# Kernel optimization log

Measured on AMD Instinct MI355X. Metric: run time of the kernel, lower is better.

Reference implementation:

```python
import jax, jax.numpy as jnp
import numpy as np

B, K, N, D = 64, 64, 32768, 2048   # batch, knn neighbors, memory size, feat dim (hardcoded 2048 in source)
NC, NHID, TOPK = 2048, 512, 5      # num clusters, gcn hidden, topk in affinity masking


def setup_inputs() -> dict:
    key = jax.random.key(0)
    ks = jax.random.split(key, 8)
    features = jax.random.normal(ks[0], (N, D), jnp.float32)
    labels = jax.random.randint(ks[1], (N,), 0, NC)
    indexes = jax.random.randint(ks[2], (B,), 0, N)
    ori_knn_neighbor = jax.random.randint(ks[3], (B, K), 0, N)
    s = 0.02
    conv_w = jax.random.normal(ks[4], (2 * D, NHID), jnp.float32) * s
    conv_b = jnp.zeros((NHID,), jnp.float32)
    w1 = jax.random.normal(ks[5], (NHID, NHID), jnp.float32) * s
    b1 = jnp.zeros((NHID,), jnp.float32)
    prelu_a = jnp.full((NHID,), 0.25, jnp.float32)
    w2 = jax.random.normal(ks[6], (NHID, 2), jnp.float32) * s
    b2 = jnp.zeros((2,), jnp.float32)
    return dict(indexes=indexes, features=features, labels=labels,
                ori_knn_neighbor=ori_knn_neighbor, conv_w=conv_w, conv_b=conv_b,
                w1=w1, b1=b1, prelu_a=prelu_a, w2=w2, b2=b2)


def _build_graphs(indexes, features, labels, ori_knn_neighbor):
    # cluster mean features (index_add_ + count normalize), done under no_grad in torch
    counts = jax.ops.segment_sum(jnp.ones((N,), jnp.float32), labels, num_segments=NC)
    clu_sum = jax.ops.segment_sum(features, labels, num_segments=NC)
    clu_mean = clu_sum / jnp.maximum(counts, 1.0)[:, None]

    def per_sample(idx, nbr):
        clu_lab = labels[nbr]                                  # [K]
        cf = clu_mean[clu_lab].at[0].set(features[idx])        # [K, D]
        A = (cf @ cf.T) / 5.0                                  # [K, K]
        j = jnp.arange(K)
        # keep only first occurrence of each cluster label (np.unique return_index)
        dup = jnp.any((clu_lab[:, None] == clu_lab[None, :]) & (j[None, :] < j[:, None]), axis=1)
        keep = (~dup).astype(A.dtype)                          # [K]
        _, ti = jax.lax.top_k(A, TOPK)                         # [K, TOPK]
        m = jnp.zeros_like(A).at[j[:, None], ti].set(1.0)
        m = ((m > 0) & (m.T > 0)).astype(A.dtype) * keep[:, None] * keep[None, :]
        A = A * m
        cf = cf / jnp.linalg.norm(cf, axis=1, keepdims=True)   # row-normalize
        cf = cf - cf[0]                                        # center on query (row 0 -> 0)
        return cf, A

    x, adj = jax.vmap(per_sample)(indexes, ori_knn_neighbor)   # [B,K,D], [B,K,K]
    return jax.lax.stop_gradient(x), jax.lax.stop_gradient(adj)


def reference(indexes, features, labels, ori_knn_neighbor,
              conv_w, conv_b, w1, b1, prelu_a, w2, b2):
    x, adj = _build_graphs(indexes, features, labels, ori_knn_neighbor)
    # GraphConv with MeanAggregator: agg = A @ x, concat, linear, relu
    agg = jnp.einsum('bij,bjd->bid', adj, x)                   # [B,K,D]
    h = jax.nn.relu(jnp.concatenate([x, agg], axis=-1) @ conv_w + conv_b)  # [B,K,NHID]
    h0 = h.reshape(-1, NHID)
    h1 = h0 @ w1 + b1
    h1 = jnp.where(h1 > 0, h1, prelu_a * h1)                   # PReLU(nhid)
    logits = h1 @ w2 + b2                                      # [B*K, 2]
    return jax.nn.softmax(logits.reshape(B, K, 2), axis=2)
```

## Files before the change

kernel.cpp:

```cpp
#include <hip/hip_runtime.h>
#include <hip/hip_bf16.h>

#define BB 64
#define KN 64
#define NPTS 32768
#define DD 2048
#define NCC 2048
#define NH 512
#define MM 4096
#define K2 4096

typedef unsigned short u16;
typedef unsigned int u32;
typedef __attribute__((ext_vector_type(8))) short short8;
typedef __attribute__((ext_vector_type(4))) float f32x4;

__device__ __forceinline__ float bf2f(u32 u){
  union { u32 i; float f; } v; v.i = u << 16; return v.f;
}
__device__ __forceinline__ u16 f2bf(float f){
  union { float f; u32 i; } v; v.f = f;
  u32 x = v.i;
  return (u16)((x + 0x7fffu + ((x >> 16) & 1u)) >> 16);
}

typedef __attribute__((address_space(3))) u32 as3_u32;
typedef const __attribute__((address_space(1))) u32 as1_u32;
__device__ __forceinline__ void glds16(const void* g, void* l){
  __builtin_amdgcn_global_load_lds((as1_u32*)g, (as3_u32*)l, 16, 0, 0);
}

__global__ void k_dtype(const u32* __restrict__ w, int* __restrict__ flag){
  __shared__ int cnt;
  if(threadIdx.x==0) cnt = 0;
  __syncthreads();
  int c = 0;
  for(int i=threadIdx.x; i<1024; i+=256){
    u32 e = (w[i] >> 7) & 0xffu;
    c += (e >= 110 && e <= 135) ? 1 : 0;
  }
  atomicAdd(&cnt, c);
  __syncthreads();
  if(threadIdx.x==0) *flag = (cnt < 512) ? 1 : 0;
}

__global__ void k_count(const int* __restrict__ labels, int* __restrict__ counts){
  int n = blockIdx.x*256 + threadIdx.x;
  atomicAdd(&counts[labels[n]], 1);
}

__global__ void k_scan(const int* __restrict__ counts, int* __restrict__ offsets){
  __shared__ int sb[256];
  int t = threadIdx.x;
  int c[8]; int s = 0;
  #pragma unroll
  for(int i=0;i<8;i++){ c[i] = counts[t*8+i]; s += c[i]; }
  sb[t] = s; __syncthreads();
  int v = s;
  for(int off=1; off<256; off<<=1){
    int u = (t>=off) ? sb[t-off] : 0;
    __syncthreads();
    v += u; sb[t] = v;
    __syncthreads();
  }
  int run = v - s;
  #pragma unroll
  for(int i=0;i<8;i++){ offsets[t*8+i] = run; run += c[i]; }
}

__global__ void k_scatter(const int* __restrict__ labels, const int* __restrict__ offsets,
                          int* __restrict__ cursor, int* __restrict__ sorted){
  int n = blockIdx.x*256 + threadIdx.x;
  int c = labels[n];
  int p = atomicAdd(&cursor[c], 1);
  sorted[offsets[c] + p] = n;
}

__global__ __launch_bounds__(256) void k_clumean(
    const void* __restrict__ feat, const int* __restrict__ counts,
    const int* __restrict__ offsets, const int* __restrict__ sorted,
    const int* __restrict__ dflag, float* __restrict__ clu){
  int c = blockIdx.x, t = threadIdx.x;
  int isf32 = *dflag;
  int cnt = counts[c], start = offsets[c];
  float acc[8] = {0,0,0,0,0,0,0,0};
  if(isf32){
    const float* ff = (const float*)feat;
    for(int r=0; r<cnt; r++){
      int row = sorted[start+r];
      const float4* p = (const float4*)(ff + (size_t)row*DD + t*8);
      float4 a = p[0], b = p[1];
      acc[0]+=a.x; acc[1]+=a.y; acc[2]+=a.z; acc[3]+=a.w;
      acc[4]+=b.x; acc[5]+=b.y; acc[6]+=b.z; acc[7]+=b.w;
    }
  } else {
    const u16* fb = (const u16*)feat;
    for(int r=0; r<cnt; r++){
      int row = sorted[start+r];
      uint4 v = *(const uint4*)(fb + (size_t)row*DD + t*8);
      acc[0]+=bf2f(v.x&0xffffu); acc[1]+=bf2f(v.x>>16);
      acc[2]+=bf2f(v.y&0xffffu); acc[3]+=bf2f(v.y>>16);
      acc[4]+=bf2f(v.z&0xffffu); acc[5]+=bf2f(v.z>>16);
      acc[6]+=bf2f(v.w&0xffffu); acc[7]+=bf2f(v.w>>16);
    }
  }
  float div = fmaxf((float)cnt, 1.0f);
  float* o = clu + (size_t)c*DD + t*8;
  #pragma unroll
  for(int i=0;i<8;i++) o[i] = acc[i] / div;
}

__global__ __launch_bounds__(64) void k_meta(
    const int* __restrict__ labels, const int* __restrict__ knn,
    int* __restrict__ lab_ws, int* __restrict__ keep_ws){
  int b = blockIdx.x, t = threadIdx.x;
  __shared__ int sl[64];
  int nbr = knn[b*64 + t];
  int lab = labels[nbr];
  sl[t] = lab; __syncthreads();
  int dup = 0;
  for(int j=0;j<t;j++) dup |= (sl[j]==lab);
  lab_ws[b*64+t] = lab;
  keep_ws[b*64+t] = dup ? 0 : 1;
}

__global__ __launch_bounds__(256) void k_Apart(
    const void* __restrict__ feat, const float* __restrict__ clu,
    const int* __restrict__ indexes, const int* __restrict__ lab_ws,
    const int* __restrict__ dflag, float* __restrict__ Apart){
  int b = blockIdx.x >> 2, g = blockIdx.x & 3;
  int t = threadIdx.x;
  __shared__ float cfT[64][68];
  __shared__ int sl[64];
  int isf32 = *dflag;
  if(t < 64) sl[t] = lab_ws[b*64 + t];
  int qidx = indexes[b];
  __syncthreads();

  int i0 = (t & 15)*4, j0 = (t >> 4)*4;
  float acc[4][4];
  #pragma unroll
  for(int a=0;a<4;a++)
    #pragma unroll
    for(int c2=0;c2<4;c2++) acc[a][c2] = 0.f;

  for(int ch=g*8; ch<g*8+8; ch++){
    int dbase = ch*64;
    #pragma unroll
    for(int ps=0; ps<16; ps++){
      int idx = ps*256 + t;
      int k = idx >> 6, dd = idx & 63;
      float v;
      if(k == 0){
        size_t fi = (size_t)qidx*DD + dbase + dd;
        v = isf32 ? ((const float*)feat)[fi] : bf2f(((const u16*)feat)[fi]);
      } else {
        v = clu[(size_t)sl[k]*DD + dbase + dd];
      }
      cfT[dd][k] = v;
    }
    __syncthreads();
    #pragma unroll 4
    for(int dd=0; dd<64; dd++){
      float4 av = *(const float4*)&cfT[dd][i0];
      float4 bv = *(const float4*)&cfT[dd][j0];
      float aa[4] = {av.x, av.y, av.z, av.w};
      float bbv[4] = {bv.x, bv.y, bv.z, bv.w};
      #pragma unroll
      for(int ii=0;ii<4;ii++)
        #pragma unroll
        for(int jj=0;jj<4;jj++)
          acc[ii][jj] += aa[ii]*bbv[jj];
    }
    __syncthreads();
  }

  float* op = Apart + ((size_t)(g*64 + b))*4096;
  #pragma unroll
  for(int ii=0;ii<4;ii++)
    *(float4*)&op[(i0+ii)*64 + j0] = make_float4(acc[ii][0], acc[ii][1], acc[ii][2], acc[ii][3]);
}

__global__ __launch_bounds__(256) void k_Afinal(
    const float* __restrict__ Apart, const int* __restrict__ keep_ws,
    float* __restrict__ adj, float* __restrict__ norms){
  int b = blockIdx.x, t = threadIdx.x;
  __shared__ float A[64][65];
  __shared__ unsigned long long mb[64];
  __shared__ int sk[64];
  const float* P = Apart + (size_t)b*4096;
  const size_t gs = (size_t)64*4096;
  #pragma unroll
  for(int ps=0; ps<16; ps++){
    int idx = ps*256 + t;
    float s = P[idx] + P[idx+gs] + P[idx+2*gs] + P[idx+3*gs];
    A[idx>>6][idx&63] = s * 0.2f;
  }
  __syncthreads();
  if(t < 64){
    unsigned long long chosen = 0;
    const float* row = A[t];
    #pragma unroll
    for(int p=0;p<5;p++){
      float best = -INFINITY; int bi = 0;
      for(int j=0;j<64;j++){
        bool taken = (chosen >> j) & 1ull;
        float v = row[j];
        if(!taken && v > best){ best = v; bi = j; }
      }
      chosen |= (1ull << bi);
    }
    mb[t] = chosen;
    sk[t] = keep_ws[b*64+t];
    norms[b*64+t] = sqrtf(fmaxf(A[t][t]*5.0f, 0.0f));
  }
  __syncthreads();
  float* O = adj + (size_t)b*4096;
  #pragma unroll
  for(int ps=0; ps<16; ps++){
    int idx = ps*256 + t;
    int i = idx >> 6, j = idx & 63;
    bool on = ((mb[i]>>j)&1ull) && ((mb[j]>>i)&1ull) && sk[i] && sk[j];
    O[idx] = on ? A[i][j] : 0.0f;
  }
}

__global__ __launch_bounds__(256) void k_xrow(
    const void* __restrict__ feat, const float* __restrict__ clu,
    const int* __restrict__ indexes, const int* __restrict__ lab_ws,
    const float* __restrict__ norms, const int* __restrict__ dflag,
    u16* __restrict__ xab){
  int r = blockIdx.x, t = threadIdx.x;
  int b = r >> 6, k = r & 63;
  size_t obase = (size_t)r*K2 + t*8;
  if(k == 0){
    *(uint4*)(xab + obase) = make_uint4(0,0,0,0);
    return;
  }
  int isf32 = *dflag;
  int qidx = indexes[b];
  float inv0 = 1.0f / fmaxf(norms[b*64], 1e-30f);
  float invk = 1.0f / fmaxf(norms[r], 1e-30f);
  float q[8];
  if(isf32){
    const float4* qp = (const float4*)((const float*)feat + (size_t)qidx*DD + t*8);
    float4 a = qp[0], bq = qp[1];
    q[0]=a.x; q[1]=a.y; q[2]=a.z; q[3]=a.w; q[4]=bq.x; q[5]=bq.y; q[6]=bq.z; q[7]=bq.w;
  } else {
    uint4 v = *(const uint4*)((const u16*)feat + (size_t)qidx*DD + t*8);
    q[0]=bf2f(v.x&0xffffu); q[1]=bf2f(v.x>>16);
    q[2]=bf2f(v.y&0xffffu); q[3]=bf2f(v.y>>16);
    q[4]=bf2f(v.z&0xffffu); q[5]=bf2f(v.z>>16);
    q[6]=bf2f(v.w&0xffffu); q[7]=bf2f(v.w>>16);
  }
  const float* cp = clu + (size_t)lab_ws[r]*DD + t*8;
  float4 c0 = *(const float4*)cp, c1 = *(const float4*)(cp+4);
  float cv[8] = {c0.x,c0.y,c0.z,c0.w,c1.x,c1.y,c1.z,c1.w};
  u16 ob[8];
  #pragma unroll
  for(int e=0;e<8;e++) ob[e] = f2bf(cv[e]*invk - q[e]*inv0);
  uint4 w;
  w.x = (u32)ob[0] | ((u32)ob[1]<<16);
  w.y = (u32)ob[2] | ((u32)ob[3]<<16);
  w.z = (u32)ob[4] | ((u32)ob[5]<<16);
  w.w = (u32)ob[6] | ((u32)ob[7]<<16);
  *(uint4*)(xab + obase) = w;
}

__global__ __launch_bounds__(256) void k_agg(
    const float* __restrict__ adj, u16* __restrict__ xab){
  int r = blockIdx.x, t = threadIdx.x; int b = r >> 6;
  __shared__ float arow[64];
  if(t < 64) arow[t] = adj[(size_t)r*64 + t];
  __syncthreads();
  float acc[8] = {0,0,0,0,0,0,0,0};
  int d = t*8;
  for(int j=0;j<64;j++){
    float s = arow[j];
    if(s != 0.0f){
      const u16* xp = xab + (size_t)(b*64+j)*K2 + d;
      uint4 v = *(const uint4*)xp;
      acc[0]+=s*bf2f(v.x&0xffffu); acc[1]+=s*bf2f(v.x>>16);
      acc[2]+=s*bf2f(v.y&0xffffu); acc[3]+=s*bf2f(v.y>>16);
      acc[4]+=s*bf2f(v.z&0xffffu); acc[5]+=s*bf2f(v.z>>16);
      acc[6]+=s*bf2f(v.w&0xffffu); acc[7]+=s*bf2f(v.w>>16);
    }
  }
  u16* o = xab + (size_t)r*K2 + DD + d;
  #pragma unroll
  for(int e=0;e<8;e++) o[e] = f2bf(acc[e]);
}

__global__ __launch_bounds__(256) void k_transpose(
    const void* __restrict__ src, u16* __restrict__ dst, int Kd, int Nd,
    const int* __restrict__ dflag){
  __shared__ u16 tile[64][65];
  int isf32 = *dflag;
  int nbt = Nd >> 6;
  int k0 = (blockIdx.x / nbt) << 6;
  int n0 = (blockIdx.x % nbt) << 6;
  int t = threadIdx.x;
  if(isf32){
    const float* s = (const float*)src;
    #pragma unroll
    for(int ph=0; ph<16; ph++){
      int idx = ph*256 + t;
      int r = idx >> 6, c = idx & 63;
      tile[r][c] = f2bf(s[(size_t)(k0+r)*Nd + n0 + c]);
    }
  } else {
    const u16* s = (const u16*)src;
    #pragma unroll
    for(int ph=0; ph<16; ph++){
      int idx = ph*256 + t;
      int r = idx >> 6, c = idx & 63;
      tile[r][c] = s[(size_t)(k0+r)*Nd + n0 + c];
    }
  }
  __syncthreads();
  #pragma unroll
  for(int ph=0; ph<16; ph++){
    int idx = ph*256 + t;
    int r = idx >> 6, c = idx & 63;
    dst[(size_t)(n0+r)*Kd + k0 + c] = tile[c][r];
  }
}

template<int EPI>
__global__ __launch_bounds__(256) void k_gemm(
    const u16* __restrict__ Am, const u16* __restrict__ Bt,
    const void* __restrict__ bias, const void* __restrict__ pa,
    const int* __restrict__ dflag,
    void* __restrict__ Cout, int Md, int Nd, int Kd)
{
  __shared__ u16 As[2][128*64];
  __shared__ u16 Bs[2][64*64];
  int isf32 = *dflag;
  int t = threadIdx.x;
  int nblk = gridDim.x;
  int bid = (blockIdx.x & 7)*(nblk >> 3) + (blockIdx.x >> 3);
  int nb = Nd >> 6;
  int m0 = (bid / nb) << 7;
  int n0 = (bid % nb) << 6;
  int wave = t >> 6, lane = t & 63;
  int wm = wave >> 1, wn = wave & 1;
  int lm = lane & 15, lq = lane >> 4;
  int lrow = lane >> 3, lcol = lane & 7;

  f32x4 acc[4][2];
  #pragma unroll
  for(int i=0;i<4;i++)
    #pragma unroll
    for(int j=0;j<2;j++) acc[i][j] = (f32x4){0.f,0.f,0.f,0.f};

  auto stage = [&](int buf, int kb){
    #pragma unroll
    for(int c=0;c<4;c++){
      int ch = wave*4 + c;
      int row = ch*8 + lrow;
      int col = lcol ^ (row & 7);
      glds16(Am + (size_t)(m0+row)*Kd + kb + col*8, &As[buf][ch*512]);
    }
    #pragma unroll
    for(int c=0;c<2;c++){
      int ch = wave*2 + c;
      int row = ch*8 + lrow;
      int col = lcol ^ (row & 7);
      glds16(Bt + (size_t)(n0+row)*Kd + kb + col*8, &Bs[buf][ch*512]);
    }
  };

  stage(0, 0);
  __syncthreads();
  int cur = 0;
  for(int kb=0; kb<Kd; kb+=64){
    if(kb + 64 < Kd) stage(cur^1, kb+64);
    #pragma unroll
    for(int kk=0;kk<2;kk++){
      short8 af[4], bfr[2];
      #pragma unroll
      for(int mi=0;mi<4;mi++){
        int r = wm*64 + mi*16 + lm;
        int p = ((kk<<2)+lq) ^ (r & 7);
        union{ uint4 u; short8 v; } x;
        x.u = *(const uint4*)&As[cur][r*64 + p*8];
        af[mi] = x.v;
      }
      #pragma unroll
      for(int ni=0;ni<2;ni++){
        int r = wn*32 + ni*16 + lm;
        int p = ((kk<<2)+lq) ^ (r & 7);
        union{ uint4 u; short8 v; } x;
        x.u = *(const uint4*)&Bs[cur][r*64 + p*8];
        bfr[ni] = x.v;
      }
      #pragma unroll
      for(int mi=0;mi<4;mi++)
        #pragma unroll
        for(int ni=0;ni<2;ni++)
          acc[mi][ni] = __builtin_amdgcn_mfma_f32_16x16x32_bf16(af[mi], bfr[ni], acc[mi][ni], 0, 0, 0);
    }
    __syncthreads();
    cur ^= 1;
  }

  #pragma unroll
  for(int ni=0;ni<2;ni++){
    int col = n0 + wn*32 + ni*16 + lm;
    float bs = isf32 ? ((const float*)bias)[col] : bf2f(((const u16*)bias)[col]);
    float av = 0.f;
    if(EPI==1) av = isf32 ? ((const float*)pa)[col] : bf2f(((const u16*)pa)[col]);
    #pragma unroll
    for(int mi=0;mi<4;mi++){
      int rowb = m0 + wm*64 + mi*16 + lq*4;
      #pragma unroll
      for(int r2=0;r2<4;r2++){
        float v = acc[mi][ni][r2] + bs;
        if(EPI==0){
          v = fmaxf(v, 0.f);
          ((u16*)Cout)[(size_t)(rowb+r2)*Nd + col] = f2bf(v);
        } else {
          v = (v > 0.f) ? v : av*v;
          ((float*)Cout)[(size_t)(rowb+r2)*Nd + col] = v;
        }
      }
    }
  }
}

__global__ __launch_bounds__(256) void k_out(
    const float* __restrict__ h1, const void* __restrict__ w2,
    const void* __restrict__ b2, const int* __restrict__ dflag,
    void* __restrict__ out){
  int t = threadIdx.x; int lane = t & 63; int row = blockIdx.x*4 + (t >> 6);
  int isf32 = *dflag;
  const float* hr = h1 + (size_t)row*NH;
  float s0 = 0.f, s1 = 0.f;
  #pragma unroll
  for(int j=0;j<NH/64;j++){
    int i = lane + j*64;
    float h = hr[i];
    float w0 = isf32 ? ((const float*)w2)[i*2+0] : bf2f(((const u16*)w2)[i*2+0]);
    float w1v= isf32 ? ((const float*)w2)[i*2+1] : bf2f(((const u16*)w2)[i*2+1]);
    s0 += h * w0;
    s1 += h * w1v;
  }
  #pragma unroll
  for(int off=32; off>0; off>>=1){
    s0 += __shfl_down(s0, off);
    s1 += __shfl_down(s1, off);
  }
  if(lane==0){
    float bb0 = isf32 ? ((const float*)b2)[0] : bf2f(((const u16*)b2)[0]);
    float bb1 = isf32 ? ((const float*)b2)[1] : bf2f(((const u16*)b2)[1]);
    float l0 = s0 + bb0;
    float l1 = s1 + bb1;
    float m = fmaxf(l0, l1);
    float e0 = expf(l0 - m), e1 = expf(l1 - m);
    float inv = 1.0f / (e0 + e1);
    if(isf32){
      ((float*)out)[row*2+0] = e0*inv;
      ((float*)out)[row*2+1] = e1*inv;
    } else {
      ((u16*)out)[row*2+0] = f2bf(e0*inv);
      ((u16*)out)[row*2+1] = f2bf(e1*inv);
    }
  }
}

__global__ void k_fill_sentinel(u32* __restrict__ out, int nwords){
  int i = blockIdx.x*256 + threadIdx.x;
  if(i < nwords) out[i] = 0x40404040u;
}

extern "C" void kernel_launch(void* const* d_in, const int* in_sizes, int n_in,
                              void* d_out, int out_size, void* d_ws, size_t ws_size,
                              hipStream_t stream) {
  const int* indexes = (const int*)d_in[0];
  const void* feat   = d_in[1];
  const int* labels  = (const int*)d_in[2];
  const int* knn     = (const int*)d_in[3];
  const void* conv_w = d_in[4];
  const void* conv_b = d_in[5];
  const void* w1     = d_in[6];
  const void* b1     = d_in[7];
  const void* pa     = d_in[8];
  const void* w2     = d_in[9];
  const void* b2     = d_in[10];

  char* w = (char*)d_ws;
  size_t o = 0;
  auto alloc = [&](size_t bytes) -> void* {
    void* p = w + o; o = (o + bytes + 255) & ~(size_t)255; return p;
  };
  int*   dflag   = (int*)  alloc(4);
  int*   counts  = (int*)  alloc((size_t)NCC*4);
  int*   cursor  = (int*)  alloc((size_t)NCC*4);
  int*   offsets = (int*)  alloc((size_t)NCC*4);
  int*   lab_ws  = (int*)  alloc((size_t)MM*4);
  int*   keep_ws = (int*)  alloc((size_t)MM*4);
  int*   sorted  = (int*)  alloc((size_t)NPTS*4);
  float* norms   = (float*)alloc((size_t)MM*4);
  float* adj     = (float*)alloc((size_t)BB*64*64*4);
  float* Apart   = (float*)alloc((size_t)4*BB*64*64*4);
  float* clu     = (float*)alloc((size_t)NCC*DD*4);
  u16*   xab     = (u16*)  alloc((size_t)MM*K2*2);
  u16*   cwT     = (u16*)  alloc((size_t)K2*NH*2);
  u16*   w1T     = (u16*)  alloc((size_t)NH*NH*2);
  u16*   hb      = (u16*)  clu;
  float* h1      = (float*)((char*)clu + (size_t)MM*NH*2);

  size_t NEED = o;
  if(ws_size < NEED){
    int nwords = out_size/2;
    k_fill_sentinel<<<(nwords+255)/256, 256, 0, stream>>>((u32*)d_out, nwords);
    return;
  }

  hipMemsetAsync(counts, 0, (size_t)NCC*4*2, stream);

  k_dtype  <<<1, 256, 0, stream>>>((const u32*)feat, dflag);
  k_count  <<<NPTS/256, 256, 0, stream>>>(labels, counts);
  k_scan   <<<1, 256, 0, stream>>>(counts, offsets);
  k_scatter<<<NPTS/256, 256, 0, stream>>>(labels, offsets, cursor, sorted);
  k_clumean<<<NCC, 256, 0, stream>>>(feat, counts, offsets, sorted, dflag, clu);
  k_meta   <<<BB, 64, 0, stream>>>(labels, knn, lab_ws, keep_ws);
  k_Apart  <<<BB*4, 256, 0, stream>>>(feat, clu, indexes, lab_ws, dflag, Apart);
  k_Afinal <<<BB, 256, 0, stream>>>(Apart, keep_ws, adj, norms);
  k_xrow   <<<MM, 256, 0, stream>>>(feat, clu, indexes, lab_ws, norms, dflag, xab);
  k_agg    <<<MM, 256, 0, stream>>>(adj, xab);

  k_transpose<<<(K2/64)*(NH/64), 256, 0, stream>>>(conv_w, cwT, K2, NH, dflag);
  k_transpose<<<(NH/64)*(NH/64), 256, 0, stream>>>(w1, w1T, NH, NH, dflag);

  k_gemm<0><<<(MM/128)*(NH/64), 256, 0, stream>>>(xab, cwT, conv_b, nullptr, dflag, (void*)hb, MM, NH, K2);
  k_gemm<1><<<(MM/128)*(NH/64), 256, 0, stream>>>(hb, w1T, b1, pa, dflag, (void*)h1, MM, NH, NH);

  k_out    <<<MM/4, 256, 0, stream>>>(h1, w2, b2, dflag, d_out);
}
```

Before: 552.9 us.

## Fuse prep kernels, skip unused cluster means, fuse xrow+agg, shrink GEMM tiles

Merges the label counting and weight transposes into one prep kernel that also marks which clusters are referenced by the knn lists. Cluster means are then computed only for used clusters, with 64-row index staging and two-row unrolling. The xrow and aggregation kernels become one kernel that builds x in LDS and uses a sparse nonzero list of adj (capped at 8 per row). GEMM tiles drop from 128x64 to 64x64 to double the block count. Dtype flags now come from input sizes on the host instead of a device probe. The 8-per-row cap assumes the top-5 mutual mask never yields more nonzeros.

```diff
diff --git a/kernel.cpp b/kernel.cpp
--- a/kernel.cpp
+++ b/kernel.cpp
@@ -30,23 +30,56 @@
   __builtin_amdgcn_global_load_lds((as1_u32*)g, (as3_u32*)l, 16, 0, 0);
 }
 
-__global__ void k_dtype(const u32* __restrict__ w, int* __restrict__ flag){
-  __shared__ int cnt;
-  if(threadIdx.x==0) cnt = 0;
-  __syncthreads();
-  int c = 0;
-  for(int i=threadIdx.x; i<1024; i+=256){
-    u32 e = (w[i] >> 7) & 0xffu;
-    c += (e >= 110 && e <= 135) ? 1 : 0;
-  }
-  atomicAdd(&cnt, c);
-  __syncthreads();
-  if(threadIdx.x==0) *flag = (cnt < 512) ? 1 : 0;
-}
-
-__global__ void k_count(const int* __restrict__ labels, int* __restrict__ counts){
-  int n = blockIdx.x*256 + threadIdx.x;
-  atomicAdd(&counts[labels[n]], 1);
+__global__ __launch_bounds__(256) void k_prep(
+    const int* __restrict__ labels, int* __restrict__ counts,
+    const int* __restrict__ knn, int* __restrict__ used,
+    const void* __restrict__ conv_w, u16* __restrict__ cwT, int fcw,
+    const void* __restrict__ w1, u16* __restrict__ w1T, int fw1){
+  __shared__ u16 tile[64][65];
+  int bb = blockIdx.x, t = threadIdx.x;
+  if(bb < 128){
+    int n = bb*256 + t;
+    atomicAdd(&counts[labels[n]], 1);
+    return;
+  }
+  if(bb == 704){
+    #pragma unroll
+    for(int i=0;i<16;i++){
+      int idx = i*256 + t;
+      used[labels[knn[idx]]] = 1;
+    }
+    return;
+  }
+  const void* src; u16* dst; int Kd, Nd, isf32, tb;
+  if(bb < 640){ src=conv_w; dst=cwT; Kd=K2; Nd=NH; isf32=fcw; tb=bb-128; }
+  else        { src=w1;     dst=w1T; Kd=NH; Nd=NH; isf32=fw1; tb=bb-640; }
+  int nbt = Nd >> 6;
+  int k0 = (tb / nbt) << 6;
+  int n0 = (tb % nbt) << 6;
+  if(isf32){
+    const float* s = (const float*)src;
+    #pragma unroll
+    for(int ph=0; ph<16; ph++){
+      int idx = ph*256 + t;
+      int r = idx >> 6, c = idx & 63;
+      tile[r][c] = f2bf(s[(size_t)(k0+r)*Nd + n0 + c]);
+    }
+  } else {
+    const u16* s = (const u16*)src;
+    #pragma unroll
+    for(int ph=0; ph<16; ph++){
+      int idx = ph*256 + t;
+      int r = idx >> 6, c = idx & 63;
+      tile[r][c] = s[(size_t)(k0+r)*Nd + n0 + c];
+    }
+  }
+  __syncthreads();
+  #pragma unroll
+  for(int ph=0; ph<16; ph++){
+    int idx = ph*256 + t;
+    int r = idx >> 6, c = idx & 63;
+    dst[(size_t)(n0+r)*Kd + k0 + c] = tile[c][r];
+  }
 }
 
 __global__ void k_scan(const int* __restrict__ counts, int* __restrict__ offsets){
@@ -79,61 +112,73 @@
 __global__ __launch_bounds__(256) void k_clumean(
     const void* __restrict__ feat, const int* __restrict__ counts,
     const int* __restrict__ offsets, const int* __restrict__ sorted,
-    const int* __restrict__ dflag, float* __restrict__ clu){
+    const int* __restrict__ used, int isf32, float* __restrict__ clu){
   int c = blockIdx.x, t = threadIdx.x;
-  int isf32 = *dflag;
+  if(!used[c]) return;
+  __shared__ int ridx[64];
   int cnt = counts[c], start = offsets[c];
   float acc[8] = {0,0,0,0,0,0,0,0};
-  if(isf32){
-    const float* ff = (const float*)feat;
-    for(int r=0; r<cnt; r++){
-      int row = sorted[start+r];
-      const float4* p = (const float4*)(ff + (size_t)row*DD + t*8);
-      float4 a = p[0], b = p[1];
-      acc[0]+=a.x; acc[1]+=a.y; acc[2]+=a.z; acc[3]+=a.w;
-      acc[4]+=b.x; acc[5]+=b.y; acc[6]+=b.z; acc[7]+=b.w;
-    }
-  } else {
-    const u16* fb = (const u16*)feat;
-    for(int r=0; r<cnt; r++){
-      int row = sorted[start+r];
-      uint4 v = *(const uint4*)(fb + (size_t)row*DD + t*8);
-      acc[0]+=bf2f(v.x&0xffffu); acc[1]+=bf2f(v.x>>16);
-      acc[2]+=bf2f(v.y&0xffffu); acc[3]+=bf2f(v.y>>16);
-      acc[4]+=bf2f(v.z&0xffffu); acc[5]+=bf2f(v.z>>16);
-      acc[6]+=bf2f(v.w&0xffffu); acc[7]+=bf2f(v.w>>16);
+  for(int base=0; base<cnt; base+=64){
+    int take = min(64, cnt-base);
+    __syncthreads();
+    if(t < take) ridx[t] = sorted[start+base+t];
+    __syncthreads();
+    if(isf32){
+      const float* ff = (const float*)feat;
+      int r = 0;
+      for(; r+2<=take; r+=2){
+        const float* p0 = ff + (size_t)ridx[r]*DD + t*8;
+        const float* p1 = ff + (size_t)ridx[r+1]*DD + t*8;
+        float4 a0=*(const float4*)p0, b0=*(const float4*)(p0+4);
+        float4 a1=*(const float4*)p1, b1=*(const float4*)(p1+4);
+        acc[0]+=a0.x+a1.x; acc[1]+=a0.y+a1.y; acc[2]+=a0.z+a1.z; acc[3]+=a0.w+a1.w;
+        acc[4]+=b0.x+b1.x; acc[5]+=b0.y+b1.y; acc[6]+=b0.z+b1.z; acc[7]+=b0.w+b1.w;
+      }
+      if(r < take){
+        const float* p0 = ff + (size_t)ridx[r]*DD + t*8;
+        float4 a0=*(const float4*)p0, b0=*(const float4*)(p0+4);
+        acc[0]+=a0.x; acc[1]+=a0.y; acc[2]+=a0.z; acc[3]+=a0.w;
+        acc[4]+=b0.x; acc[5]+=b0.y; acc[6]+=b0.z; acc[7]+=b0.w;
+      }
+    } else {
+      const u16* fb = (const u16*)feat;
+      int r = 0;
+      for(; r+2<=take; r+=2){
+        const u16* p0 = fb + (size_t)ridx[r]*DD + t*8;
+        const u16* p1 = fb + (size_t)ridx[r+1]*DD + t*8;
+        uint4 v0 = *(const uint4*)p0, v1 = *(const uint4*)p1;
+        acc[0]+=bf2f(v0.x&0xffffu)+bf2f(v1.x&0xffffu); acc[1]+=bf2f(v0.x>>16)+bf2f(v1.x>>16);
+        acc[2]+=bf2f(v0.y&0xffffu)+bf2f(v1.y&0xffffu); acc[3]+=bf2f(v0.y>>16)+bf2f(v1.y>>16);
+        acc[4]+=bf2f(v0.z&0xffffu)+bf2f(v1.z&0xffffu); acc[5]+=bf2f(v0.z>>16)+bf2f(v1.z>>16);
+        acc[6]+=bf2f(v0.w&0xffffu)+bf2f(v1.w&0xffffu); acc[7]+=bf2f(v0.w>>16)+bf2f(v1.w>>16);
+      }
+      if(r < take){
+        const u16* p0 = fb + (size_t)ridx[r]*DD + t*8;
+        uint4 v0 = *(const uint4*)p0;
+        acc[0]+=bf2f(v0.x&0xffffu); acc[1]+=bf2f(v0.x>>16);
+        acc[2]+=bf2f(v0.y&0xffffu); acc[3]+=bf2f(v0.y>>16);
+        acc[4]+=bf2f(v0.z&0xffffu); acc[5]+=bf2f(v0.z>>16);
+        acc[6]+=bf2f(v0.w&0xffffu); acc[7]+=bf2f(v0.w>>16);
+      }
     }
   }
   float div = fmaxf((float)cnt, 1.0f);
   float* o = clu + (size_t)c*DD + t*8;
-  #pragma unroll
-  for(int i=0;i<8;i++) o[i] = acc[i] / div;
-}
-
-__global__ __launch_bounds__(64) void k_meta(
-    const int* __restrict__ labels, const int* __restrict__ knn,
-    int* __restrict__ lab_ws, int* __restrict__ keep_ws){
-  int b = blockIdx.x, t = threadIdx.x;
-  __shared__ int sl[64];
-  int nbr = knn[b*64 + t];
-  int lab = labels[nbr];
-  sl[t] = lab; __syncthreads();
-  int dup = 0;
-  for(int j=0;j<t;j++) dup |= (sl[j]==lab);
-  lab_ws[b*64+t] = lab;
-  keep_ws[b*64+t] = dup ? 0 : 1;
+  float4 o0 = make_float4(acc[0]/div, acc[1]/div, acc[2]/div, acc[3]/div);
+  float4 o1 = make_float4(acc[4]/div, acc[5]/div, acc[6]/div, acc[7]/div);
+  *(float4*)o = o0;
+  *(float4*)(o+4) = o1;
 }
 
 __global__ __launch_bounds__(256) void k_Apart(
     const void* __restrict__ feat, const float* __restrict__ clu,
-    const int* __restrict__ indexes, const int* __restrict__ lab_ws,
-    const int* __restrict__ dflag, float* __restrict__ Apart){
+    const int* __restrict__ indexes, const int* __restrict__ labels,
+    const int* __restrict__ knn, int isf32, float* __restrict__ Apart){
   int b = blockIdx.x >> 2, g = blockIdx.x & 3;
   int t = threadIdx.x;
   __shared__ float cfT[64][68];
   __shared__ int sl[64];
-  int isf32 = *dflag;
-  if(t < 64) sl[t] = lab_ws[b*64 + t];
+  if(t < 64) sl[t] = labels[knn[b*64 + t]];
   int qidx = indexes[b];
   __syncthreads();
 
@@ -182,12 +227,15 @@
 }
 
 __global__ __launch_bounds__(256) void k_Afinal(
-    const float* __restrict__ Apart, const int* __restrict__ keep_ws,
+    const float* __restrict__ Apart, const int* __restrict__ labels,
+    const int* __restrict__ knn,
     float* __restrict__ adj, float* __restrict__ norms){
   int b = blockIdx.x, t = threadIdx.x;
   __shared__ float A[64][65];
   __shared__ unsigned long long mb[64];
+  __shared__ int sl[64];
   __shared__ int sk[64];
+  if(t < 64) sl[t] = labels[knn[b*64 + t]];
   const float* P = Apart + (size_t)b*4096;
   const size_t gs = (size_t)64*4096;
   #pragma unroll
@@ -198,6 +246,9 @@
   }
   __syncthreads();
   if(t < 64){
+    int dup = 0;
+    for(int j=0;j<t;j++) dup |= (sl[j]==sl[t]);
+    sk[t] = dup ? 0 : 1;
     unsigned long long chosen = 0;
     const float* row = A[t];
     #pragma unroll
@@ -211,7 +262,6 @@
       chosen |= (1ull << bi);
     }
     mb[t] = chosen;
-    sk[t] = keep_ws[b*64+t];
     norms[b*64+t] = sqrtf(fmaxf(A[t][t]*5.0f, 0.0f));
   }
   __syncthreads();
@@ -225,148 +275,119 @@
   }
 }
 
-__global__ __launch_bounds__(256) void k_xrow(
+__global__ __launch_bounds__(256) void k_xagg(
     const void* __restrict__ feat, const float* __restrict__ clu,
-    const int* __restrict__ indexes, const int* __restrict__ lab_ws,
-    const float* __restrict__ norms, const int* __restrict__ dflag,
-    u16* __restrict__ xab){
-  int r = blockIdx.x, t = threadIdx.x;
-  int b = r >> 6, k = r & 63;
-  size_t obase = (size_t)r*K2 + t*8;
-  if(k == 0){
-    *(uint4*)(xab + obase) = make_uint4(0,0,0,0);
-    return;
-  }
-  int isf32 = *dflag;
+    const int* __restrict__ indexes, const int* __restrict__ labels,
+    const int* __restrict__ knn, const float* __restrict__ norms,
+    const float* __restrict__ adj, int isf32, u16* __restrict__ xab){
+  int b = blockIdx.x >> 2, g = blockIdx.x & 3;
+  int t = threadIdx.x;
+  __shared__ u16  xs[64][512];
+  __shared__ float adjs[64][65];
+  __shared__ float nzv[64][8];
+  __shared__ u16   nzj[64][8];
+  __shared__ int   nzc[64];
+  __shared__ int   sl[64];
+  __shared__ float sn[64];
+
+  const float* Ab = adj + (size_t)b*4096;
+  #pragma unroll
+  for(int ps=0; ps<16; ps++){
+    int idx = ps*256 + t;
+    adjs[idx>>6][idx&63] = Ab[idx];
+  }
+  if(t < 64){
+    sl[t] = labels[knn[b*64 + t]];
+    sn[t] = 1.0f / fmaxf(norms[b*64 + t], 1e-30f);
+  }
   int qidx = indexes[b];
-  float inv0 = 1.0f / fmaxf(norms[b*64], 1e-30f);
-  float invk = 1.0f / fmaxf(norms[r], 1e-30f);
-  float q[8];
+  int d = g*512 + t*2;
+  float q0, q1;
   if(isf32){
-    const float4* qp = (const float4*)((const float*)feat + (size_t)qidx*DD + t*8);
-    float4 a = qp[0], bq = qp[1];
-    q[0]=a.x; q[1]=a.y; q[2]=a.z; q[3]=a.w; q[4]=bq.x; q[5]=bq.y; q[6]=bq.z; q[7]=bq.w;
+    float2 qv = *(const float2*)((const float*)feat + (size_t)qidx*DD + d);
+    q0 = qv.x; q1 = qv.y;
   } else {
-    uint4 v = *(const uint4*)((const u16*)feat + (size_t)qidx*DD + t*8);
-    q[0]=bf2f(v.x&0xffffu); q[1]=bf2f(v.x>>16);
-    q[2]=bf2f(v.y&0xffffu); q[3]=bf2f(v.y>>16);
-    q[4]=bf2f(v.z&0xffffu); q[5]=bf2f(v.z>>16);
-    q[6]=bf2f(v.w&0xffffu); q[7]=bf2f(v.w>>16);
-  }
-  const float* cp = clu + (size_t)lab_ws[r]*DD + t*8;
-  float4 c0 = *(const float4*)cp, c1 = *(const float4*)(cp+4);
-  float cv[8] = {c0.x,c0.y,c0.z,c0.w,c1.x,c1.y,c1.z,c1.w};
-  u16 ob[8];
-  #pragma unroll
-  for(int e=0;e<8;e++) ob[e] = f2bf(cv[e]*invk - q[e]*inv0);
-  uint4 w;
-  w.x = (u32)ob[0] | ((u32)ob[1]<<16);
-  w.y = (u32)ob[2] | ((u32)ob[3]<<16);
-  w.z = (u32)ob[4] | ((u32)ob[5]<<16);
-  w.w = (u32)ob[6] | ((u32)ob[7]<<16);
-  *(uint4*)(xab + obase) = w;
-}
-
-__global__ __launch_bounds__(256) void k_agg(
-    const float* __restrict__ adj, u16* __restrict__ xab){
-  int r = blockIdx.x, t = threadIdx.x; int b = r >> 6;
-  __shared__ float arow[64];
-  if(t < 64) arow[t] = adj[(size_t)r*64 + t];
-  __syncthreads();
-  float acc[8] = {0,0,0,0,0,0,0,0};
-  int d = t*8;
-  for(int j=0;j<64;j++){
-    float s = arow[j];
-    if(s != 0.0f){
-      const u16* xp = xab + (size_t)(b*64+j)*K2 + d;
-      uint4 v = *(const uint4*)xp;
-      acc[0]+=s*bf2f(v.x&0xffffu); acc[1]+=s*bf2f(v.x>>16);
-      acc[2]+=s*bf2f(v.y&0xffffu); acc[3]+=s*bf2f(v.y>>16);
-      acc[4]+=s*bf2f(v.z&0xffffu); acc[5]+=s*bf2f(v.z>>16);
-      acc[6]+=s*bf2f(v.w&0xffffu); acc[7]+=s*bf2f(v.w>>16);
-    }
-  }
-  u16* o = xab + (size_t)r*K2 + DD + d;
-  #pragma unroll
-  for(int e=0;e<8;e++) o[e] = f2bf(acc[e]);
-}
-
-__global__ __launch_bounds__(256) void k_transpose(
-    const void* __restrict__ src, u16* __restrict__ dst, int Kd, int Nd,
-    const int* __restrict__ dflag){
-  __shared__ u16 tile[64][65];
-  int isf32 = *dflag;
-  int nbt = Nd >> 6;
-  int k0 = (blockIdx.x / nbt) << 6;
-  int n0 = (blockIdx.x % nbt) << 6;
-  int t = threadIdx.x;
-  if(isf32){
-    const float* s = (const float*)src;
-    #pragma unroll
-    for(int ph=0; ph<16; ph++){
-      int idx = ph*256 + t;
-      int r = idx >> 6, c = idx & 63;
-      tile[r][c] = f2bf(s[(size_t)(k0+r)*Nd + n0 + c]);
-    }
-  } else {
-    const u16* s = (const u16*)src;
-    #pragma unroll
-    for(int ph=0; ph<16; ph++){
-      int idx = ph*256 + t;
-      int r = idx >> 6, c = idx & 63;
-      tile[r][c] = s[(size_t)(k0+r)*Nd + n0 + c];
-    }
-  }
-  __syncthreads();
-  #pragma unroll
-  for(int ph=0; ph<16; ph++){
-    int idx = ph*256 + t;
-    int r = idx >> 6, c = idx & 63;
-    dst[(size_t)(n0+r)*Kd + k0 + c] = tile[c][r];
+    u32 w = *(const u32*)((const u16*)feat + (size_t)qidx*DD + d);
+    q0 = bf2f(w & 0xffffu); q1 = bf2f(w >> 16);
+  }
+  __syncthreads();
+  if(t < 64){
+    int c = 0;
+    for(int j=0;j<64;j++){
+      float v = adjs[t][j];
+      if(v != 0.0f && c < 8){ nzv[t][c] = v; nzj[t][c] = (u16)j; c++; }
+    }
+    nzc[t] = c;
+  }
+  float inv0 = sn[0];
+  q0 *= inv0; q1 *= inv0;
+
+  *(u32*)&xs[0][t*2] = 0u;
+  *(u32*)(xab + (size_t)(b*64)*K2 + d) = 0u;
+  for(int k=1;k<64;k++){
+    float2 cv = *(const float2*)(clu + (size_t)sl[k]*DD + d);
+    float invk = sn[k];
+    u16 x0 = f2bf(cv.x*invk - q0), x1 = f2bf(cv.y*invk - q1);
+    u32 w = (u32)x0 | ((u32)x1 << 16);
+    *(u32*)&xs[k][t*2] = w;
+    *(u32*)(xab + (size_t)(b*64+k)*K2 + d) = w;
+  }
+  __syncthreads();
+
+  for(int r=0;r<64;r++){
+    float a0 = 0.f, a1 = 0.f;
+    int c = nzc[r];
+    for(int p=0;p<c;p++){
+      float s = nzv[r][p]; int j = nzj[r][p];
+      u32 w = *(const u32*)&xs[j][t*2];
+      a0 += s*bf2f(w & 0xffffu);
+      a1 += s*bf2f(w >> 16);
+    }
+    u32 w = (u32)f2bf(a0) | ((u32)f2bf(a1) << 16);
+    *(u32*)(xab + (size_t)(b*64+r)*K2 + DD + d) = w;
   }
 }
 
 template<int EPI>
-__global__ __launch_bounds__(256) void k_gemm(
+__global__ __launch_bounds__(256, 2) void k_gemm(
     const u16* __restrict__ Am, const u16* __restrict__ Bt,
     const void* __restrict__ bias, const void* __restrict__ pa,
-    const int* __restrict__ dflag,
+    int fbias, int fpa,
     void* __restrict__ Cout, int Md, int Nd, int Kd)
 {
-  __shared__ u16 As[2][128*64];
+  __shared__ u16 As[2][64*64];
   __shared__ u16 Bs[2][64*64];
-  int isf32 = *dflag;
   int t = threadIdx.x;
   int nblk = gridDim.x;
   int bid = (blockIdx.x & 7)*(nblk >> 3) + (blockIdx.x >> 3);
   int nb = Nd >> 6;
-  int m0 = (bid / nb) << 7;
+  int m0 = (bid / nb) << 6;
   int n0 = (bid % nb) << 6;
   int wave = t >> 6, lane = t & 63;
   int wm = wave >> 1, wn = wave & 1;
   int lm = lane & 15, lq = lane >> 4;
   int lrow = lane >> 3, lcol = lane & 7;
 
-  f32x4 acc[4][2];
-  #pragma unroll
-  for(int i=0;i<4;i++)
+  f32x4 acc[2][2];
+  #pragma unroll
+  for(int i=0;i<2;i++)
     #pragma unroll
     for(int j=0;j<2;j++) acc[i][j] = (f32x4){0.f,0.f,0.f,0.f};
 
   auto stage = [&](int buf, int kb){
     #pragma unroll
-    for(int c=0;c<4;c++){
-      int ch = wave*4 + c;
-      int row = ch*8 + lrow;
+    for(int c=0;c<2;c++){
+      int cb = wave*2 + c;
+      int row = cb*8 + lrow;
       int col = lcol ^ (row & 7);
-      glds16(Am + (size_t)(m0+row)*Kd + kb + col*8, &As[buf][ch*512]);
+      glds16(Am + (size_t)(m0+row)*Kd + kb + col*8, &As[buf][cb*512]);
     }
     #pragma unroll
     for(int c=0;c<2;c++){
-      int ch = wave*2 + c;
-      int row = ch*8 + lrow;
+      int cb = wave*2 + c;
+      int row = cb*8 + lrow;
       int col = lcol ^ (row & 7);
-      glds16(Bt + (size_t)(n0+row)*Kd + kb + col*8, &Bs[buf][ch*512]);
+      glds16(Bt + (size_t)(n0+row)*Kd + kb + col*8, &Bs[buf][cb*512]);
     }
   };
 
@@ -377,10 +398,10 @@
     if(kb + 64 < Kd) stage(cur^1, kb+64);
     #pragma unroll
     for(int kk=0;kk<2;kk++){
-      short8 af[4], bfr[2];
+      short8 af[2], bfr[2];
       #pragma unroll
-      for(int mi=0;mi<4;mi++){
-        int r = wm*64 + mi*16 + lm;
+      for(int mi=0;mi<2;mi++){
+        int r = wm*32 + mi*16 + lm;
         int p = ((kk<<2)+lq) ^ (r & 7);
         union{ uint4 u; short8 v; } x;
         x.u = *(const uint4*)&As[cur][r*64 + p*8];
@@ -395,7 +416,7 @@
         bfr[ni] = x.v;
       }
       #pragma unroll
-      for(int mi=0;mi<4;mi++)
+      for(int mi=0;mi<2;mi++)
         #pragma unroll
         for(int ni=0;ni<2;ni++)
           acc[mi][ni] = __builtin_amdgcn_mfma_f32_16x16x32_bf16(af[mi], bfr[ni], acc[mi][ni], 0, 0, 0);
@@ -407,12 +428,12 @@
   #pragma unroll
   for(int ni=0;ni<2;ni++){
     int col = n0 + wn*32 + ni*16 + lm;
-    float bs = isf32 ? ((const float*)bias)[col] : bf2f(((const u16*)bias)[col]);
+    float bs = fbias ? ((const float*)bias)[col] : bf2f(((const u16*)bias)[col]);
     float av = 0.f;
-    if(EPI==1) av = isf32 ? ((const float*)pa)[col] : bf2f(((const u16*)pa)[col]);
-    #pragma unroll
-    for(int mi=0;mi<4;mi++){
-      int rowb = m0 + wm*64 + mi*16 + lq*4;
+    if(EPI==1) av = fpa ? ((const float*)pa)[col] : bf2f(((const u16*)pa)[col]);
+    #pragma unroll
+    for(int mi=0;mi<2;mi++){
+      int rowb = m0 + wm*32 + mi*16 + lq*4;
       #pragma unroll
       for(int r2=0;r2<4;r2++){
         float v = acc[mi][ni][r2] + bs;
@@ -430,18 +451,17 @@
 
 __global__ __launch_bounds__(256) void k_out(
     const float* __restrict__ h1, const void* __restrict__ w2,
-    const void* __restrict__ b2, const int* __restrict__ dflag,
+    const void* __restrict__ b2, int fw2, int fb2, int fo,
     void* __restrict__ out){
   int t = threadIdx.x; int lane = t & 63; int row = blockIdx.x*4 + (t >> 6);
-  int isf32 = *dflag;
   const float* hr = h1 + (size_t)row*NH;
   float s0 = 0.f, s1 = 0.f;
   #pragma unroll
   for(int j=0;j<NH/64;j++){
     int i = lane + j*64;
     float h = hr[i];
-    float w0 = isf32 ? ((const float*)w2)[i*2+0] : bf2f(((const u16*)w2)[i*2+0]);
-    float w1v= isf32 ? ((const float*)w2)[i*2+1] : bf2f(((const u16*)w2)[i*2+1]);
+    float w0 = fw2 ? ((const float*)w2)[i*2+0] : bf2f(((const u16*)w2)[i*2+0]);
+    float w1v= fw2 ? ((const float*)w2)[i*2+1] : bf2f(((const u16*)w2)[i*2+1]);
     s0 += h * w0;
     s1 += h * w1v;
   }
@@ -451,14 +471,14 @@
     s1 += __shfl_down(s1, off);
   }
   if(lane==0){
-    float bb0 = isf32 ? ((const float*)b2)[0] : bf2f(((const u16*)b2)[0]);
-    float bb1 = isf32 ? ((const float*)b2)[1] : bf2f(((const u16*)b2)[1]);
+    float bb0 = fb2 ? ((const float*)b2)[0] : bf2f(((const u16*)b2)[0]);
+    float bb1 = fb2 ? ((const float*)b2)[1] : bf2f(((const u16*)b2)[1]);
     float l0 = s0 + bb0;
     float l1 = s1 + bb1;
     float m = fmaxf(l0, l1);
     float e0 = expf(l0 - m), e1 = expf(l1 - m);
     float inv = 1.0f / (e0 + e1);
-    if(isf32){
+    if(fo){
       ((float*)out)[row*2+0] = e0*inv;
       ((float*)out)[row*2+1] = e1*inv;
     } else {
@@ -488,17 +508,25 @@
   const void* w2     = d_in[9];
   const void* b2     = d_in[10];
 
+  int ff  = (in_sizes[1]  != (int)((size_t)NPTS*DD*2));
+  int fcw = (in_sizes[4]  != (int)((size_t)2*DD*NH*2));
+  int fcb = (in_sizes[5]  != NH*2);
+  int fw1 = (in_sizes[6]  != (int)((size_t)NH*NH*2));
+  int fb1 = (in_sizes[7]  != NH*2);
+  int fpa = (in_sizes[8]  != NH*2);
+  int fw2 = (in_sizes[9]  != NH*2*2);
+  int fb2 = (in_sizes[10] != 2*2);
+  int fo  = (out_size     != MM*2*2);
+
   char* w = (char*)d_ws;
   size_t o = 0;
   auto alloc = [&](size_t bytes) -> void* {
     void* p = w + o; o = (o + bytes + 255) & ~(size_t)255; return p;
   };
-  int*   dflag   = (int*)  alloc(4);
   int*   counts  = (int*)  alloc((size_t)NCC*4);
   int*   cursor  = (int*)  alloc((size_t)NCC*4);
+  int*   used    = (int*)  alloc((size_t)NCC*4);
   int*   offsets = (int*)  alloc((size_t)NCC*4);
-  int*   lab_ws  = (int*)  alloc((size_t)MM*4);
-  int*   keep_ws = (int*)  alloc((size_t)MM*4);
   int*   sorted  = (int*)  alloc((size_t)NPTS*4);
   float* norms   = (float*)alloc((size_t)MM*4);
   float* adj     = (float*)alloc((size_t)BB*64*64*4);
@@ -512,29 +540,23 @@
 
   size_t NEED = o;
   if(ws_size < NEED){
-    int nwords = out_size/2;
+    int nwords = out_size/4;
     k_fill_sentinel<<<(nwords+255)/256, 256, 0, stream>>>((u32*)d_out, nwords);
     return;
   }
 
-  hipMemsetAsync(counts, 0, (size_t)NCC*4*2, stream);
-
-  k_dtype  <<<1, 256, 0, stream>>>((const u32*)feat, dflag);
-  k_count  <<<NPTS/256, 256, 0, stream>>>(labels, counts);
+  hipMemsetAsync(counts, 0, (size_t)NCC*4*3, stream);
+
+  k_prep   <<<705, 256, 0, stream>>>(labels, counts, knn, used, conv_w, cwT, fcw, w1, w1T, fw1);
   k_scan   <<<1, 256, 0, stream>>>(counts, offsets);
   k_scatter<<<NPTS/256, 256, 0, stream>>>(labels, offsets, cursor, sorted);
-  k_clumean<<<NCC, 256, 0, stream>>>(feat, counts, offsets, sorted, dflag, clu);
-  k_meta   <<<BB, 64, 0, stream>>>(labels, knn, lab_ws, keep_ws);
-  k_Apart  <<<BB*4, 256, 0, stream>>>(feat, clu, indexes, lab_ws, dflag, Apart);
-  k_Afinal <<<BB, 256, 0, stream>>>(Apart, keep_ws, adj, norms);
-  k_xrow   <<<MM, 256, 0, stream>>>(feat, clu, indexes, lab_ws, norms, dflag, xab);
-  k_agg    <<<MM, 256, 0, stream>>>(adj, xab);
-
-  k_transpose<<<(K2/64)*(NH/64), 256, 0, stream>>>(conv_w, cwT, K2, NH, dflag);
-  k_transpose<<<(NH/64)*(NH/64), 256, 0, stream>>>(w1, w1T, NH, NH, dflag);
-
-  k_gemm<0><<<(MM/128)*(NH/64), 256, 0, stream>>>(xab, cwT, conv_b, nullptr, dflag, (void*)hb, MM, NH, K2);
-  k_gemm<1><<<(MM/128)*(NH/64), 256, 0, stream>>>(hb, w1T, b1, pa, dflag, (void*)h1, MM, NH, NH);
-
-  k_out    <<<MM/4, 256, 0, stream>>>(h1, w2, b2, dflag, d_out);
-}
+  k_clumean<<<NCC, 256, 0, stream>>>(feat, counts, offsets, sorted, used, ff, clu);
+  k_Apart  <<<BB*4, 256, 0, stream>>>(feat, clu, indexes, labels, knn, ff, Apart);
+  k_Afinal <<<BB, 256, 0, stream>>>(Apart, labels, knn, adj, norms);
+  k_xagg   <<<BB*4, 256, 0, stream>>>(feat, clu, indexes, labels, knn, norms, adj, ff, xab);
+
+  k_gemm<0><<<(MM/64)*(NH/64), 256, 0, stream>>>(xab, cwT, conv_b, nullptr, fcb, 0, (void*)hb, MM, NH, K2);
+  k_gemm<1><<<(MM/64)*(NH/64), 256, 0, stream>>>(hb, w1T, b1, pa, fb1, fpa, (void*)h1, MM, NH, NH);
+
+  k_out    <<<MM/4, 256, 0, stream>>>(h1, w2, b2, fw2, fb2, fo, d_out);
+}
```

Result: no change. 558.8 us (+1.1%).
